# Optimization experiments

Measured on AMD Instinct MI355X. Metric: run time of the kernel, lower is better.

Reference implementation:

```python
import jax, jax.numpy as jnp
import numpy as np

HID = 64      # hidden_size of message MLP
NF = 20       # n_node_features
EF = 20       # n_edge_features
ITERS = 3
N_ENV, N_NODES, N_EDGES = 16, 5000, 50000


def setup_inputs() -> dict:
    key = jax.random.key(0)
    ks = jax.random.split(key, 12)
    s = 0.1
    node_features = jax.random.normal(ks[0], (N_ENV, N_NODES, NF), jnp.float32)
    edges = jax.random.randint(ks[1], (2, N_EDGES), 0, N_NODES, dtype=jnp.int32)
    # msg_net: Linear(2*NF,HID) -> Tanh -> Linear(HID,HID) -> Tanh -> Linear(HID,EF)
    W1 = jax.random.normal(ks[2], (HID, 2 * NF), jnp.float32) * s
    b1 = jax.random.normal(ks[3], (HID,), jnp.float32) * s
    W2 = jax.random.normal(ks[4], (HID, HID), jnp.float32) * s
    b2 = jax.random.normal(ks[5], (HID,), jnp.float32) * s
    W3 = jax.random.normal(ks[6], (EF, HID), jnp.float32) * s
    b3 = jax.random.normal(ks[7], (EF,), jnp.float32) * s
    # GRU(input=EF, hidden=NF): weight_ih (3*NF, EF), weight_hh (3*NF, NF)
    Wih = jax.random.normal(ks[8], (3 * NF, EF), jnp.float32) * s
    Whh = jax.random.normal(ks[9], (3 * NF, NF), jnp.float32) * s
    b_ih = jax.random.normal(ks[10], (3 * NF,), jnp.float32) * s
    b_hh = jax.random.normal(ks[11], (3 * NF,), jnp.float32) * s
    return {"node_features": node_features, "edges": edges,
            "W1": W1, "b1": b1, "W2": W2, "b2": b2, "W3": W3, "b3": b3,
            "Wih": Wih, "Whh": Whh, "b_ih": b_ih, "b_hh": b_hh}


def reference(node_features, edges, W1, b1, W2, b2, W3, b3, Wih, Whh, b_ih, b_hh):
    n_env, n_nodes, _ = node_features.shape
    # Bidirectionalize edges: cat([edges, edges[[1,0]]], dim=1)
    e = jnp.concatenate([edges, edges[::-1]], axis=1)  # (2, 2E)
    src, dst = e[0], e[1]
    for _ in range(ITERS):
        # gather src/dst node feats -> message MLP
        x = jnp.concatenate([node_features[:, src], node_features[:, dst]], axis=2)  # (env, 2E, 2*NF)
        h = jnp.tanh(x @ W1.T + b1)
        h = jnp.tanh(h @ W2.T + b2)
        msg = h @ W3.T + b3  # (env, 2E, EF)
        # scatter-add messages to source nodes
        store = jnp.zeros((n_env, n_nodes, EF), node_features.dtype).at[:, src].add(msg)
        # single-step GRU update (seq_len=1, h0=node_features), vectorized over env & node
        gi = store @ Wih.T + b_ih           # (env, nodes, 3*NF)
        gh = node_features @ Whh.T + b_hh   # (env, nodes, 3*NF)
        ir, iz, in_ = jnp.split(gi, 3, axis=-1)
        hr, hz, hn = jnp.split(gh, 3, axis=-1)
        r = jax.nn.sigmoid(ir + hr)
        z = jax.nn.sigmoid(iz + hz)
        n = jnp.tanh(in_ + r * hn)
        node_features = (1.0 - z) * n + z * node_features
    return node_features
```

## Files before the change

kernel.cpp:

```cpp
#include <hip/hip_runtime.h>

#define NFEAT 20
#define EFEAT 20
#define HID   64
#define NENV  16
#define NNODES 5000
#define NEDGES 50000
#define E2 (2*NEDGES)
#define ITERS 3
#define ROWS 64
#define THREADS 128
#define NPAD 24

typedef __attribute__((ext_vector_type(8))) _Float16 f16x8;
typedef __attribute__((ext_vector_type(2))) __fp16  h16x2;
typedef __attribute__((ext_vector_type(4))) float f32x4;

__device__ __forceinline__ ushort f2h(float f) {
    _Float16 h = (_Float16)f;
    return *(ushort*)&h;
}
__device__ __forceinline__ unsigned pk2h(float a, float b) {
    h16x2 p = __builtin_amdgcn_cvt_pkrtz(a, b);
    return *(unsigned*)&p;
}
__device__ __forceinline__ float fast_tanh(float x) {
    float e = __builtin_exp2f(x * 2.8853900817779268f);
    float r = __builtin_amdgcn_rcpf(e + 1.f);
    return fmaf(-2.f, r, 1.f);
}
__device__ __forceinline__ float fast_sigmoid(float x) {
    float e = __builtin_exp2f(x * -1.4426950408889634f);
    return __builtin_amdgcn_rcpf(1.f + e);
}

__global__ __launch_bounds__(256) void hist_kernel(const int* __restrict__ edges,
                                                   int* __restrict__ cnt) {
    int e = blockIdx.x * 256 + threadIdx.x;
    if (e < E2) atomicAdd(&cnt[edges[e]], 1);
}

__global__ __launch_bounds__(256) void scan_kernel(const int* __restrict__ cnt,
                                                   int* __restrict__ cursor) {
    __shared__ int part[256];
    int t = threadIdx.x;
    int local[20]; int s = 0;
    int base = t * 20;
    #pragma unroll
    for (int i = 0; i < 20; i++) {
        int idx = base + i;
        int v = (idx < NNODES) ? cnt[idx] : 0;
        local[i] = s; s += v;
    }
    part[t] = s;
    __syncthreads();
    for (int d = 1; d < 256; d <<= 1) {
        int v = (t >= d) ? part[t - d] : 0;
        __syncthreads();
        part[t] += v;
        __syncthreads();
    }
    int excl = part[t] - s;
    #pragma unroll
    for (int i = 0; i < 20; i++) {
        int idx = base + i;
        if (idx < NNODES) cursor[idx] = excl + local[i];
    }
}

__global__ __launch_bounds__(256) void scatter_kernel(const int* __restrict__ edges,
                                                      int* __restrict__ cursor,
                                                      int* __restrict__ snode,
                                                      int* __restrict__ dnode) {
    int e = blockIdx.x * 256 + threadIdx.x;
    if (e < E2) {
        int s = edges[e];
        int di = e + NEDGES; if (di >= E2) di -= E2;
        int d = edges[di];
        int pos = atomicAdd(&cursor[s], 1);
        snode[pos] = s;
        dnode[pos] = d;
    }
}

__global__ void prep_weights(const float* __restrict__ W1, const float* __restrict__ W2,
                             const float* __restrict__ W3,
                             ushort* __restrict__ W1p, ushort* __restrict__ W2p,
                             ushort* __restrict__ W3p) {
    int t = threadIdx.x;
    for (int i = t; i < 64 * 64; i += 256) {
        int n = i >> 6, k = i & 63;
        float v = 0.f;
        if (k < NFEAT)                          v = W1[n * (2 * NFEAT) + k];
        else if (k >= NPAD && k < NPAD + NFEAT) v = W1[n * (2 * NFEAT) + NFEAT + (k - NPAD)];
        W1p[i] = f2h(v);
    }
    for (int i = t; i < 64 * 64; i += 256)
        W2p[i] = f2h(W2[i]);
    for (int i = t; i < 32 * 64; i += 256) {
        int n = i >> 6, k = i & 63;
        W3p[i] = (n < EFEAT) ? f2h(W3[n * HID + k]) : (ushort)0;
    }
}

__global__ __launch_bounds__(256) void conv_nf(const float* __restrict__ nf,
                                               ushort* __restrict__ nfp) {
    int gid = blockIdx.x * 256 + threadIdx.x;
    if (gid >= NENV * NNODES) return;
    const float* p = nf + (size_t)gid * NFEAT;
    ushort* ph = nfp + (size_t)gid * NPAD;
    #pragma unroll
    for (int k = 0; k < NFEAT; k++) ph[k] = f2h(p[k]);
    *(uint2*)(ph + NFEAT) = make_uint2(0u, 0u);
}

__global__ __launch_bounds__(THREADS) void edge_mlp_mfma(
    const ushort* __restrict__ nfp,
    const int*   __restrict__ snode, const int* __restrict__ dnode,
    const ushort* __restrict__ W1p, const ushort* __restrict__ W2p,
    const ushort* __restrict__ W3p,
    const float* __restrict__ b1, const float* __restrict__ b2,
    const float* __restrict__ b3,
    float* __restrict__ store)
{
    __shared__ ushort smem16[4096];
    ushort* Hp = smem16;
    float*  msgf = (float*)smem16;
    int*    msgi = (int*)smem16;

    const int tid  = threadIdx.x;
    const int wave = tid >> 6;
    const int lane = tid & 63;
    const int lr   = lane & 15;
    const int kg   = lane >> 4;
    const int m0   = wave * 32;

#define MFMA2(acc, w0, w1, x0, x1)                                                  \
    acc = __builtin_amdgcn_mfma_f32_16x16x32_f16(w0, x0, acc, 0, 0, 0);             \
    acc = __builtin_amdgcn_mfma_f32_16x16x32_f16(w1, x1, acc, 0, 0, 0);

#define STORE_H4(accv, m_, rr_)                                                     \
    {                                                                               \
        float t0 = fast_tanh(accv[0]), t1 = fast_tanh(accv[1]);                     \
        float t2 = fast_tanh(accv[2]), t3 = fast_tanh(accv[3]);                     \
        unsigned p01 = pk2h(t0, t1), p23 = pk2h(t2, t3);                            \
        int c8 = (m_) * 2 + (kg >> 1);                                              \
        int idx = (rr_) * 64 + ((c8 ^ ((rr_) & 7)) << 3) + ((kg & 1) << 2);         \
        *(uint2*)(Hp + idx) = make_uint2(p01, p23);                                 \
    }

    {
        f16x8 wp[4][2];
        f32x4 bb[4];
        #pragma unroll
        for (int m = 0; m < 4; m++) {
            #pragma unroll
            for (int kt = 0; kt < 2; kt++)
                wp[m][kt] = *(const f16x8*)(W1p + (m * 16 + lr) * 64 + kt * 32 + kg * 8);
            bb[m] = *(const f32x4*)(b1 + m * 16 + kg * 4);
        }
        #pragma unroll
        for (int n = 0; n < 2; n++) {
            int rr = m0 + n * 16 + lr;
            int gr = blockIdx.x * ROWS + rr;
            int env = gr / E2;
            int sr  = gr - env * E2;
            const ushort* sp_ = nfp + (size_t)(env * NNODES + snode[sr]) * NPAD;
            const ushort* dp_ = nfp + (size_t)(env * NNODES + dnode[sr]) * NPAD;
            f16x8 x0, x1;
            if (kg < 3) x0 = *(const f16x8*)(sp_ + kg * 8);
            else        x0 = *(const f16x8*)(dp_);
            if (kg < 2) x1 = *(const f16x8*)(dp_ + 8 + kg * 8);
            else        x1 = f16x8{(_Float16)0,(_Float16)0,(_Float16)0,(_Float16)0,
                                   (_Float16)0,(_Float16)0,(_Float16)0,(_Float16)0};
            f32x4 acc[4];
            #pragma unroll
            for (int m = 0; m < 4; m++) {
                acc[m] = bb[m];
                MFMA2(acc[m], wp[m][0], wp[m][1], x0, x1)
            }
            #pragma unroll
            for (int m = 0; m < 4; m++) STORE_H4(acc[m], m, rr)
        }
    }

    {
        f16x8 wp[4][2];
        f32x4 bb[4];
        #pragma unroll
        for (int m = 0; m < 4; m++) {
            #pragma unroll
            for (int kt = 0; kt < 2; kt++)
                wp[m][kt] = *(const f16x8*)(W2p + (m * 16 + lr) * 64 + kt * 32 + kg * 8);
            bb[m] = *(const f32x4*)(b2 + m * 16 + kg * 4);
        }
        #pragma unroll
        for (int n = 0; n < 2; n++) {
            int rr = m0 + n * 16 + lr, sw = rr & 7;
            f16x8 x0 = *(const f16x8*)(Hp + rr * 64 + ((kg ^ sw) << 3));
            f16x8 x1 = *(const f16x8*)(Hp + rr * 64 + (((4 + kg) ^ sw) << 3));
            f32x4 acc[4];
            #pragma unroll
            for (int m = 0; m < 4; m++) {
                acc[m] = bb[m];
                MFMA2(acc[m], wp[m][0], wp[m][1], x0, x1)
            }
            #pragma unroll
            for (int m = 0; m < 4; m++) STORE_H4(acc[m], m, rr)
        }
    }

    {
        int i_ = lane & 31;
        int gr_i  = blockIdx.x * ROWS + m0 + i_;
        int env_i = gr_i / E2;
        int sr_i  = gr_i - env_i * E2;
        int key   = env_i * NNODES + snode[sr_i];

        f16x8 w3[2][2];
        #pragma unroll
        for (int m = 0; m < 2; m++)
            #pragma unroll
            for (int kt = 0; kt < 2; kt++)
                w3[m][kt] = *(const f16x8*)(W3p + (m * 16 + lr) * 64 + kt * 32 + kg * 8);
        f32x4 bb0 = *(const f32x4*)(b3 + kg * 4);
        f32x4 bb1 = (kg == 0) ? *(const f32x4*)(b3 + 16)
                              : f32x4{0.f, 0.f, 0.f, 0.f};

        f16x8 xb[2][2];
        #pragma unroll
        for (int n = 0; n < 2; n++) {
            int rr = m0 + n * 16 + lr, sw = rr & 7;
            xb[n][0] = *(const f16x8*)(Hp + rr * 64 + ((kg ^ sw) << 3));
            xb[n][1] = *(const f16x8*)(Hp + rr * 64 + (((4 + kg) ^ sw) << 3));
        }
        f32x4 acc0[2], acc1[2];
        #pragma unroll
        for (int n = 0; n < 2; n++) {
            acc0[n] = bb0;
            MFMA2(acc0[n], w3[0][0], w3[0][1], xb[n][0], xb[n][1])
            acc1[n] = bb1;
            MFMA2(acc1[n], w3[1][0], w3[1][1], xb[n][0], xb[n][1])
        }

        int wbase = wave * 1024;
        #pragma unroll
        for (int n = 0; n < 2; n++) {
            int row = n * 16 + lr;
            int g0 = kg ^ (row & 7);
            *(f32x4*)(msgf + wbase + row * 32 + (g0 << 2)) = acc0[n];
            if (kg == 0) {
                int g1 = 4 ^ (row & 7);
                *(f32x4*)(msgf + wbase + row * 32 + (g1 << 2)) = acc1[n];
            }
        }
        if (lane < 32) msgi[wbase + i_ * 32 + ((5 ^ (i_ & 7)) << 2)] = key;

        int nxt = __shfl_down(key, 1);
        bool flag = (i_ == 31) || (key != nxt);
        unsigned fm = (unsigned)__ballot(flag);

        if (lane < EFEAT) {
            int c = lane, g = c >> 2, o = c & 3;
            float sum = 0.f;
            for (int i = 0; i < 32; i++) {
                sum += msgf[wbase + i * 32 + ((g ^ (i & 7)) << 2) + o];
                if ((fm >> i) & 1u) {
                    int curk = msgi[wbase + i * 32 + ((5 ^ (i & 7)) << 2)];
                    atomicAdd(store + (size_t)curk * EFEAT + c, sum);
                    sum = 0.f;
                }
            }
        }
    }
#undef STORE_H4
#undef MFMA2
}

__global__ __launch_bounds__(256) void gru_kernel(
    const float* __restrict__ store,
    const float* __restrict__ Wih, const float* __restrict__ bih,
    const float* __restrict__ Whh, const float* __restrict__ bhh,
    float* __restrict__ nf,
    ushort* __restrict__ nfp)
{
    int gid = blockIdx.x * blockDim.x + threadIdx.x;
    const int total = NENV * NNODES;
    if (gid >= total) return;

    const float* s = store + (size_t)gid * EFEAT;
    float*       h = nf    + (size_t)gid * NFEAT;
    ushort*     ph = nfp   + (size_t)gid * NPAD;

    float sv[EFEAT], hv[NFEAT];
    #pragma unroll
    for (int k = 0; k < EFEAT; k++) sv[k] = s[k];
    #pragma unroll
    for (int k = 0; k < NFEAT; k++) hv[k] = h[k];

    for (int t = 0; t < NFEAT; t++) {
        float ir = bih[t],            hr = bhh[t];
        float iz = bih[NFEAT + t],    hz = bhh[NFEAT + t];
        float in_ = bih[2*NFEAT + t], hn = bhh[2*NFEAT + t];
        const float* wr = Wih + t * EFEAT;
        const float* wz = Wih + (NFEAT + t) * EFEAT;
        const float* wn = Wih + (2*NFEAT + t) * EFEAT;
        #pragma unroll
        for (int k = 0; k < EFEAT; k++) {
            ir  = fmaf(sv[k], wr[k], ir);
            iz  = fmaf(sv[k], wz[k], iz);
            in_ = fmaf(sv[k], wn[k], in_);
        }
        const float* vr = Whh + t * NFEAT;
        const float* vz = Whh + (NFEAT + t) * NFEAT;
        const float* vn = Whh + (2*NFEAT + t) * NFEAT;
        #pragma unroll
        for (int k = 0; k < NFEAT; k++) {
            hr = fmaf(hv[k], vr[k], hr);
            hz = fmaf(hv[k], vz[k], hz);
            hn = fmaf(hv[k], vn[k], hn);
        }
        float r = fast_sigmoid(ir + hr);
        float z = fast_sigmoid(iz + hz);
        float n = fast_tanh(in_ + r * hn);
        float hw = (1.f - z) * n + z * hv[t];
        h[t] = hw;
        ph[t] = f2h(hw);
    }
    *(uint2*)(ph + NFEAT) = make_uint2(0u, 0u);
}

extern "C" void kernel_launch(void* const* d_in, const int* in_sizes, int n_in,
                              void* d_out, int out_size, void* d_ws, size_t ws_size,
                              hipStream_t stream) {
    const float* nf_in = (const float*)d_in[0];
    const int*   edges = (const int*)d_in[1];
    const float* W1 = (const float*)d_in[2];
    const float* b1 = (const float*)d_in[3];
    const float* W2 = (const float*)d_in[4];
    const float* b2 = (const float*)d_in[5];
    const float* W3 = (const float*)d_in[6];
    const float* b3 = (const float*)d_in[7];
    const float* Wih = (const float*)d_in[8];
    const float* Whh = (const float*)d_in[9];
    const float* bih = (const float*)d_in[10];
    const float* bhh = (const float*)d_in[11];

    float* nf    = (float*)d_out;
    float* store = (float*)d_ws;
    const size_t nf_bytes    = (size_t)NENV * NNODES * NFEAT * sizeof(float);
    const size_t store_bytes = (size_t)NENV * NNODES * EFEAT * sizeof(float);
    ushort* W1p = (ushort*)((char*)d_ws + store_bytes);
    ushort* W2p = W1p + 64 * 64;
    ushort* W3p = W2p + 64 * 64;
    ushort* nfp = W3p + 32 * 64;
    int* cnt    = (int*)(nfp + (size_t)NENV * NNODES * NPAD);
    int* cursor = cnt + NNODES;
    int* snode  = cursor + NNODES;
    int* dnode  = snode + E2;

    prep_weights<<<1, 256, 0, stream>>>(W1, W2, W3, W1p, W2p, W3p);
    conv_nf<<<(NENV * NNODES + 255) / 256, 256, 0, stream>>>(nf_in, nfp);
    hipMemcpyAsync(nf, nf_in, nf_bytes, hipMemcpyDeviceToDevice, stream);
    hipMemsetAsync(cnt, 0, NNODES * sizeof(int), stream);
    hist_kernel<<<(E2 + 255) / 256, 256, 0, stream>>>(edges, cnt);
    scan_kernel<<<1, 256, 0, stream>>>(cnt, cursor);
    scatter_kernel<<<(E2 + 255) / 256, 256, 0, stream>>>(edges, cursor, snode, dnode);

    const int edge_blocks = (NENV * E2) / ROWS;
    dim3 grid_n((NENV * NNODES + 255) / 256);

    for (int it = 0; it < ITERS; it++) {
        hipMemsetAsync(store, 0, store_bytes, stream);
        edge_mlp_mfma<<<edge_blocks, THREADS, 0, stream>>>(nfp, snode, dnode,
                                                           W1p, W2p, W3p,
                                                           b1, b2, b3, store);
        gru_kernel<<<grid_n, 256, 0, stream>>>(store, Wih, bih, Whh, bhh, nf, nfp);
    }
}
```

Before: 567.4 us.

## Segmented-reduce edge messages in registers via shuffles; split GRU outputs across two threads

The per-wave scatter of edge messages no longer stages them in shared memory and runs a serial 20-lane loop. Messages now stay in MFMA accumulator registers, and a shuffle-based segmented scan over equal destination keys combines them. One lane per run then issues the atomics, which spreads atomic issue across lanes and drops LDS traffic, at the cost of many shuffles. The GRU kernel now uses two threads per node, each computing half of the output features, which doubles thread-level parallelism but repeats the input loads.

```diff
diff --git a/kernel.cpp b/kernel.cpp
--- a/kernel.cpp
+++ b/kernel.cpp
@@ -23,6 +23,12 @@
 __device__ __forceinline__ unsigned pk2h(float a, float b) {
     h16x2 p = __builtin_amdgcn_cvt_pkrtz(a, b);
     return *(unsigned*)&p;
+}
+__device__ __forceinline__ f32x4 shfl4(f32x4 v, int src) {
+    f32x4 r;
+    r[0] = __shfl(v[0], src); r[1] = __shfl(v[1], src);
+    r[2] = __shfl(v[2], src); r[3] = __shfl(v[3], src);
+    return r;
 }
 __device__ __forceinline__ float fast_tanh(float x) {
     float e = __builtin_exp2f(x * 2.8853900817779268f);
@@ -123,10 +129,7 @@
     const float* __restrict__ b3,
     float* __restrict__ store)
 {
-    __shared__ ushort smem16[4096];
-    ushort* Hp = smem16;
-    float*  msgf = (float*)smem16;
-    int*    msgi = (int*)smem16;
+    __shared__ ushort Hp[4096];
 
     const int tid  = threadIdx.x;
     const int wave = tid >> 6;
@@ -211,11 +214,12 @@
     }
 
     {
-        int i_ = lane & 31;
-        int gr_i  = blockIdx.x * ROWS + m0 + i_;
-        int env_i = gr_i / E2;
-        int sr_i  = gr_i - env_i * E2;
-        int key   = env_i * NNODES + snode[sr_i];
+        int gr0  = blockIdx.x * ROWS + m0 + lr;
+        int env0 = gr0 / E2, sr0 = gr0 - env0 * E2;
+        int k0   = env0 * NNODES + snode[sr0];
+        int gr1  = gr0 + 16;
+        int env1 = gr1 / E2, sr1 = gr1 - env1 * E2;
+        int k1   = env1 * NNODES + snode[sr1];
 
         f16x8 w3[2][2];
         #pragma unroll
@@ -227,49 +231,62 @@
         f32x4 bb1 = (kg == 0) ? *(const f32x4*)(b3 + 16)
                               : f32x4{0.f, 0.f, 0.f, 0.f};
 
-        f16x8 xb[2][2];
-        #pragma unroll
-        for (int n = 0; n < 2; n++) {
-            int rr = m0 + n * 16 + lr, sw = rr & 7;
-            xb[n][0] = *(const f16x8*)(Hp + rr * 64 + ((kg ^ sw) << 3));
-            xb[n][1] = *(const f16x8*)(Hp + rr * 64 + (((4 + kg) ^ sw) << 3));
-        }
-        f32x4 acc0[2], acc1[2];
-        #pragma unroll
-        for (int n = 0; n < 2; n++) {
-            acc0[n] = bb0;
-            MFMA2(acc0[n], w3[0][0], w3[0][1], xb[n][0], xb[n][1])
-            acc1[n] = bb1;
-            MFMA2(acc1[n], w3[1][0], w3[1][1], xb[n][0], xb[n][1])
-        }
-
-        int wbase = wave * 1024;
-        #pragma unroll
-        for (int n = 0; n < 2; n++) {
-            int row = n * 16 + lr;
-            int g0 = kg ^ (row & 7);
-            *(f32x4*)(msgf + wbase + row * 32 + (g0 << 2)) = acc0[n];
+        f32x4 s0, s1, t0, t1;
+        {
+            int rr = m0 + lr, sw = rr & 7;
+            f16x8 x0 = *(const f16x8*)(Hp + rr * 64 + ((kg ^ sw) << 3));
+            f16x8 x1 = *(const f16x8*)(Hp + rr * 64 + (((4 + kg) ^ sw) << 3));
+            s0 = bb0; MFMA2(s0, w3[0][0], w3[0][1], x0, x1)
+            s1 = bb1; MFMA2(s1, w3[1][0], w3[1][1], x0, x1)
+        }
+        {
+            int rr = m0 + 16 + lr, sw = rr & 7;
+            f16x8 x0 = *(const f16x8*)(Hp + rr * 64 + ((kg ^ sw) << 3));
+            f16x8 x1 = *(const f16x8*)(Hp + rr * 64 + (((4 + kg) ^ sw) << 3));
+            t0 = bb0; MFMA2(t0, w3[0][0], w3[0][1], x0, x1)
+            t1 = bb1; MFMA2(t1, w3[1][0], w3[1][1], x0, x1)
+        }
+
+        #pragma unroll
+        for (int d = 1; d < 16; d <<= 1) {
+            int src = (lr >= d) ? (lane - d) : lane;
+            int pk0 = __shfl(k0, src);
+            f32x4 p0 = shfl4(s0, src), p1 = shfl4(s1, src);
+            if ((lr >= d) && (pk0 == k0)) { s0 += p0; s1 += p1; }
+            int pk1 = __shfl(k1, src);
+            f32x4 q0 = shfl4(t0, src), q1 = shfl4(t1, src);
+            if ((lr >= d) && (pk1 == k1)) { t0 += q0; t1 += q1; }
+        }
+        {
+            int l15 = lane | 15;
+            int bk  = __shfl(k0, l15);
+            f32x4 c0 = shfl4(s0, l15), c1 = shfl4(s1, l15);
+            if (k1 == bk) { t0 += c0; t1 += c1; }
+        }
+        int nk0  = __shfl(k0, lane + 1);
+        int bk10 = __shfl(k1, lane & ~15);
+        bool end0 = (lr < 15) ? (k0 != nk0) : (k0 != bk10);
+        int nk1  = __shfl(k1, lane + 1);
+        bool end1 = (lr == 15) || (k1 != nk1);
+
+        if (end0) {
+            float* sp = store + (size_t)k0 * EFEAT + (kg << 2);
+            atomicAdd(sp + 0, s0[0]); atomicAdd(sp + 1, s0[1]);
+            atomicAdd(sp + 2, s0[2]); atomicAdd(sp + 3, s0[3]);
             if (kg == 0) {
-                int g1 = 4 ^ (row & 7);
-                *(f32x4*)(msgf + wbase + row * 32 + (g1 << 2)) = acc1[n];
+                float* sq = store + (size_t)k0 * EFEAT + 16;
+                atomicAdd(sq + 0, s1[0]); atomicAdd(sq + 1, s1[1]);
+                atomicAdd(sq + 2, s1[2]); atomicAdd(sq + 3, s1[3]);
             }
         }
-        if (lane < 32) msgi[wbase + i_ * 32 + ((5 ^ (i_ & 7)) << 2)] = key;
-
-        int nxt = __shfl_down(key, 1);
-        bool flag = (i_ == 31) || (key != nxt);
-        unsigned fm = (unsigned)__ballot(flag);
-
-        if (lane < EFEAT) {
-            int c = lane, g = c >> 2, o = c & 3;
-            float sum = 0.f;
-            for (int i = 0; i < 32; i++) {
-                sum += msgf[wbase + i * 32 + ((g ^ (i & 7)) << 2) + o];
-                if ((fm >> i) & 1u) {
-                    int curk = msgi[wbase + i * 32 + ((5 ^ (i & 7)) << 2)];
-                    atomicAdd(store + (size_t)curk * EFEAT + c, sum);
-                    sum = 0.f;
-                }
+        if (end1) {
+            float* sp = store + (size_t)k1 * EFEAT + (kg << 2);
+            atomicAdd(sp + 0, t0[0]); atomicAdd(sp + 1, t0[1]);
+            atomicAdd(sp + 2, t0[2]); atomicAdd(sp + 3, t0[3]);
+            if (kg == 0) {
+                float* sq = store + (size_t)k1 * EFEAT + 16;
+                atomicAdd(sq + 0, t1[0]); atomicAdd(sq + 1, t1[1]);
+                atomicAdd(sq + 2, t1[2]); atomicAdd(sq + 3, t1[3]);
             }
         }
     }
@@ -284,13 +301,12 @@
     float* __restrict__ nf,
     ushort* __restrict__ nfp)
 {
-    int gid = blockIdx.x * blockDim.x + threadIdx.x;
-    const int total = NENV * NNODES;
-    if (gid >= total) return;
-
-    const float* s = store + (size_t)gid * EFEAT;
-    float*       h = nf    + (size_t)gid * NFEAT;
-    ushort*     ph = nfp   + (size_t)gid * NPAD;
+    int gid  = blockIdx.x * 256 + threadIdx.x;
+    int node = gid >> 1, half = gid & 1;
+
+    const float* s = store + (size_t)node * EFEAT;
+    float*       h = nf    + (size_t)node * NFEAT;
+    ushort*     ph = nfp   + (size_t)node * NPAD;
 
     float sv[EFEAT], hv[NFEAT];
     #pragma unroll
@@ -298,7 +314,10 @@
     #pragma unroll
     for (int k = 0; k < NFEAT; k++) hv[k] = h[k];
 
-    for (int t = 0; t < NFEAT; t++) {
+    __syncthreads();
+
+    const int t0 = half * (NFEAT / 2), t1 = t0 + NFEAT / 2;
+    for (int t = t0; t < t1; t++) {
         float ir = bih[t],            hr = bhh[t];
         float iz = bih[NFEAT + t],    hz = bhh[NFEAT + t];
         float in_ = bih[2*NFEAT + t], hn = bhh[2*NFEAT + t];
@@ -327,7 +346,7 @@
         h[t] = hw;
         ph[t] = f2h(hw);
     }
-    *(uint2*)(ph + NFEAT) = make_uint2(0u, 0u);
+    if (half) *(uint2*)(ph + NFEAT) = make_uint2(0u, 0u);
 }
 
 extern "C" void kernel_launch(void* const* d_in, const int* in_sizes, int n_in,
@@ -368,13 +387,13 @@
     scatter_kernel<<<(E2 + 255) / 256, 256, 0, stream>>>(edges, cursor, snode, dnode);
 
     const int edge_blocks = (NENV * E2) / ROWS;
-    dim3 grid_n((NENV * NNODES + 255) / 256);
+    dim3 grid_g((NENV * NNODES * 2) / 256);
 
     for (int it = 0; it < ITERS; it++) {
         hipMemsetAsync(store, 0, store_bytes, stream);
         edge_mlp_mfma<<<edge_blocks, THREADS, 0, stream>>>(nfp, snode, dnode,
                                                            W1p, W2p, W3p,
                                                            b1, b2, b3, store);
-        gru_kernel<<<grid_n, 256, 0, stream>>>(store, Wih, bih, Whh, bhh, nf, nfp);
-    }
-}
+        gru_kernel<<<grid_g, 256, 0, stream>>>(store, Wih, bih, Whh, bhh, nf, nfp);
+    }
+}
```

Measured after the change: 638.7 us. 1.13x slower.
